# Performance work log

Hardware: AMD Instinct MI355X
Metric: run time of the kernel (lower is better)

Reference implementation:

```python
import jax, jax.numpy as jnp
import numpy as np

N_HEADS = 8
TANH_CLIP = 10.0


def setup_inputs() -> dict:
    key = jax.random.key(0)
    ks = jax.random.split(key, 7)
    B, N, D = 128, 1000, 512
    embeddings = jax.random.normal(ks[0], (B, N, D), dtype=jnp.float32)
    step_context = jax.random.normal(ks[1], (B, 1, 2 * D), dtype=jnp.float32)
    # action mask: True = feasible action; guarantee at least one feasible per row
    action_mask = jax.random.uniform(ks[2], (B, 1, N)) > 0.3
    action_mask = action_mask.at[:, :, 0].set(True)
    s = 0.02
    W_node = jax.random.normal(ks[3], (D, 3 * D), dtype=jnp.float32) * s
    W_fixed = jax.random.normal(ks[4], (D, D), dtype=jnp.float32) * s
    W_step = jax.random.normal(ks[5], (2 * D, D), dtype=jnp.float32) * s
    W_out = jax.random.normal(ks[6], (D, D), dtype=jnp.float32) * s
    return {"embeddings": embeddings, "step_context": step_context,
            "action_mask": action_mask, "W_node": W_node, "W_fixed": W_fixed,
            "W_step": W_step, "W_out": W_out}


def reference(embeddings, step_context, action_mask, W_node, W_fixed, W_step, W_out):
    B, N, D = embeddings.shape
    H = N_HEADS
    hd = D // H
    neg_inf = jnp.float32(-jnp.inf)

    # --- precompute (Decoder._precompute) ---
    graph_embed = embeddings.mean(axis=1)                      # [B, D]
    kvl = embeddings @ W_node                                  # [B, N, 3D]
    _gk, gv, logit_key = jnp.split(kvl, 3, axis=-1)
    # source bug: glimpse_key variable is overwritten with glimpse_val, and
    # attention is called with key = value = glimpse_val
    KV = gv.reshape(B, N, H, hd).transpose(0, 2, 1, 3)         # [B, H, N, hd]
    graph_context = (graph_embed @ W_fixed)[:, None, :]        # [B, 1, D]

    # --- per-step query (Decoder._get_log_p) ---
    query = graph_context + step_context @ W_step              # [B, 1, D]
    q = query.reshape(B, 1, H, hd).transpose(0, 2, 1, 3)       # [B, H, 1, hd]

    # --- inner MHA (scaled_dot_product_attention with boolean mask) ---
    scores = jnp.einsum('bhqs,bhns->bhqn', q, KV) / jnp.sqrt(jnp.float32(hd))
    scores = jnp.where(action_mask[:, None, :, :], scores, neg_inf)  # [B,H,1,N]
    attn = jax.nn.softmax(scores, axis=-1)
    heads = jnp.einsum('bhqn,bhns->bhqs', attn, KV)            # [B, H, 1, hd]
    heads = heads.transpose(0, 2, 1, 3).reshape(B, 1, D)       # [B, 1, D]

    # --- glimpse projection and logit head ---
    glimpse = heads @ W_out                                    # [B, 1, D]
    logits = jnp.einsum('bqd,bnd->bqn', glimpse, logit_key) / jnp.sqrt(jnp.float32(D))
    logits = jnp.tanh(logits) * TANH_CLIP
    logits = jnp.where(action_mask, logits, neg_inf)
    return jax.nn.log_softmax(logits, axis=-1)                 # [B, 1, N]
```

## Files before the change

kernel.cpp:

```cpp
#include <hip/hip_runtime.h>
#include <math.h>

#define B 128
#define N 1000
#define D 512
#define H 8
#define NCHUNK 8
#define CHUNK 125
#define CG_N 10
#define SUBR 25
#define NSUB 4
#define ESW 516

#define OFF_PMEAN   0
#define OFF_QW      (OFF_PMEAN + B*NCHUNK*D)
#define OFF_PAE     (OFF_QW + B*D*H)
#define OFF_MC      (OFF_PAE + B*CG_N*H*D)
#define OFF_ZC      (OFF_MC + B*CG_N*H)
#define OFF_GW      (OFF_ZC + B*CG_N*H)
#define OFF_LG      (OFF_GW + B*D)
#define OFF_LMAX    (OFF_LG + B*N)
#define OFF_LSUM    (OFF_LMAX + B*NCHUNK)

__global__ void k1_partial_mean(const float* __restrict__ emb, float* __restrict__ ws){
    int chunk = blockIdx.x, b = blockIdx.y, t = threadIdx.x;
    const float4* e4 = (const float4*)emb;
    float4 acc = make_float4(0.f, 0.f, 0.f, 0.f);
    size_t rowbase = ((size_t)b * N + (size_t)chunk * CHUNK) * (D / 4);
    for (int n = 0; n < CHUNK; ++n) {
        float4 v = e4[rowbase + (size_t)n * (D / 4) + t];
        acc.x += v.x; acc.y += v.y; acc.z += v.z; acc.w += v.w;
    }
    float4* o = (float4*)(ws + OFF_PMEAN + (size_t)(b * NCHUNK + chunk) * D);
    o[t] = acc;
}

__global__ void k2_prep(const float* __restrict__ stepc, const float* __restrict__ Wnode,
                        const float* __restrict__ Wfix, const float* __restrict__ Wstep,
                        float* __restrict__ ws){
    int b = blockIdx.x, d = threadIdx.x;
    __shared__ float ge[D];
    __shared__ float q[D];
    float s = 0.f;
    #pragma unroll
    for (int c = 0; c < NCHUNK; ++c) s += ws[OFF_PMEAN + (size_t)(b * NCHUNK + c) * D + d];
    ge[d] = s * (1.0f / N);
    __syncthreads();
    float a0 = 0.f, a1 = 0.f, a2 = 0.f, a3 = 0.f;
    for (int k = 0; k < D; k += 4) {
        a0 = fmaf(ge[k],     Wfix[(size_t)k * D + d],       a0);
        a1 = fmaf(ge[k + 1], Wfix[(size_t)(k + 1) * D + d], a1);
        a2 = fmaf(ge[k + 2], Wfix[(size_t)(k + 2) * D + d], a2);
        a3 = fmaf(ge[k + 3], Wfix[(size_t)(k + 3) * D + d], a3);
    }
    const float* sc = stepc + (size_t)b * 2 * D;
    for (int k = 0; k < 2 * D; k += 4) {
        a0 = fmaf(sc[k],     Wstep[(size_t)k * D + d],       a0);
        a1 = fmaf(sc[k + 1], Wstep[(size_t)(k + 1) * D + d], a1);
        a2 = fmaf(sc[k + 2], Wstep[(size_t)(k + 2) * D + d], a2);
        a3 = fmaf(sc[k + 3], Wstep[(size_t)(k + 3) * D + d], a3);
    }
    q[d] = (a0 + a1) + (a2 + a3);
    __syncthreads();
    const float* wrow = Wnode + (size_t)d * 3 * D + D;
    float* outp = ws + OFF_QW + ((size_t)b * D + d) * H;
    #pragma unroll
    for (int h = 0; h < H; ++h) {
        float a = 0.f;
        const float* qh = q + h * 64;
        const float* wh = wrow + h * 64;
        #pragma unroll 8
        for (int s2 = 0; s2 < 64; ++s2) a = fmaf(qh[s2], wh[s2], a);
        outp[h] = a;
    }
}

__global__ __launch_bounds__(512) void kc_attn(const float* __restrict__ emb,
        const unsigned char* __restrict__ mask, float* __restrict__ ws){
    const int cg = blockIdx.x, b = blockIdx.y, t = threadIdx.x;
    __shared__ float es[SUBR * ESW];
    __shared__ float ps[16 * H * 32];
    __shared__ float sc[H * 32];
    __shared__ float pp[H * 32];
    __shared__ float mrun[H], zrun[H], ff[H];
    float acc[H];
    #pragma unroll
    for (int h = 0; h < H; ++h) acc[h] = 0.f;
    if (t < H) { mrun[t] = -INFINITY; zrun[t] = 0.f; }
    __syncthreads();
    const float* qw = ws + OFF_QW + (size_t)b * D * H;
    const int n_b = t & 31, dblk = t >> 5;
    for (int sub = 0; sub < NSUB; ++sub) {
        const int row0 = cg * (NSUB * SUBR) + sub * SUBR;
        const float4* e4 = (const float4*)(emb + ((size_t)b * N + row0) * D);
        #pragma unroll
        for (int r = 0; r < 7; ++r) {
            int idx = r * 512 + t;
            if (idx < SUBR * (D / 4)) {
                float4 v = e4[idx];
                int i = idx >> 7, c = idx & 127;
                *(float4*)&es[i * ESW + c * 4] = v;
            }
        }
        __syncthreads();
        {
            float a[H];
            #pragma unroll
            for (int h = 0; h < H; ++h) a[h] = 0.f;
            if (n_b < SUBR) {
                const float* er = es + n_b * ESW + dblk * 32;
                const float* qd = qw + (size_t)(dblk * 32) * H;
                #pragma unroll 8
                for (int dd = 0; dd < 32; ++dd) {
                    float e = er[dd];
                    float4 q0 = *(const float4*)(qd + dd * 8);
                    float4 q1 = *(const float4*)(qd + dd * 8 + 4);
                    a[0] = fmaf(e, q0.x, a[0]); a[1] = fmaf(e, q0.y, a[1]);
                    a[2] = fmaf(e, q0.z, a[2]); a[3] = fmaf(e, q0.w, a[3]);
                    a[4] = fmaf(e, q1.x, a[4]); a[5] = fmaf(e, q1.y, a[5]);
                    a[6] = fmaf(e, q1.z, a[6]); a[7] = fmaf(e, q1.w, a[7]);
                }
            }
            #pragma unroll
            for (int h = 0; h < H; ++h) ps[(dblk * H + h) * 32 + n_b] = a[h];
        }
        __syncthreads();
        if (t < 256) {
            int h = t >> 5, n = t & 31;
            float s = -INFINITY;
            if (n < SUBR) {
                float v = 0.f;
                #pragma unroll
                for (int k = 0; k < 16; ++k) v += ps[(k * H + h) * 32 + n];
                bool m = mask[(size_t)b * N + row0 + n] != 0;
                s = m ? v * 0.125f : -INFINITY;
            }
            sc[h * 32 + n] = s;
        }
        __syncthreads();
        if (t < 256) {
            int h = t >> 5, j = t & 31;
            float v = sc[h * 32 + j];
            float gm = v;
            #pragma unroll
            for (int o = 16; o > 0; o >>= 1) gm = fmaxf(gm, __shfl_xor(gm, o));
            float mold = mrun[h];
            float mnew = fmaxf(mold, gm);
            float p = (mnew == -INFINITY) ? 0.f : __expf(v - mnew);
            pp[h * 32 + j] = p;
            float zc = p;
            #pragma unroll
            for (int o = 16; o > 0; o >>= 1) zc += __shfl_xor(zc, o);
            if (j == 0) {
                float f = (mnew == -INFINITY) ? 1.f : __expf(mold - mnew);
                ff[h] = f;
                mrun[h] = mnew;
                zrun[h] = zrun[h] * f + zc;
            }
        }
        __syncthreads();
        #pragma unroll
        for (int h = 0; h < H; ++h) acc[h] *= ff[h];
        for (int i = 0; i < SUBR; ++i) {
            float e = es[i * ESW + t];
            #pragma unroll
            for (int h = 0; h < H; ++h) acc[h] = fmaf(pp[h * 32 + i], e, acc[h]);
        }
        __syncthreads();
    }
    float* paeb = ws + OFF_PAE + (((size_t)b * CG_N + cg) * H) * (size_t)D;
    #pragma unroll
    for (int h = 0; h < H; ++h) paeb[(size_t)h * D + t] = acc[h];
    if (t < H) {
        ws[OFF_MC + ((size_t)b * CG_N + cg) * H + t] = mrun[t];
        ws[OFF_ZC + ((size_t)b * CG_N + cg) * H + t] = zrun[t];
    }
}

__global__ __launch_bounds__(512) void kd_post(const float* __restrict__ Wnode,
        const float* __restrict__ Wout, float* __restrict__ ws){
    int b = blockIdx.x, t = threadIdx.x;
    __shared__ float ae[H * D];
    __shared__ float heads[D];
    __shared__ float gl[D];
    __shared__ float wgt[CG_N * H], iZ[H];
    if (t < H) {
        float M = -INFINITY;
        for (int c = 0; c < CG_N; ++c)
            M = fmaxf(M, ws[OFF_MC + ((size_t)b * CG_N + c) * H + t]);
        float Z = 0.f;
        for (int c = 0; c < CG_N; ++c) {
            float m = ws[OFF_MC + ((size_t)b * CG_N + c) * H + t];
            float w = (m == -INFINITY) ? 0.f : __expf(m - M);
            wgt[c * H + t] = w;
            Z += w * ws[OFF_ZC + ((size_t)b * CG_N + c) * H + t];
        }
        iZ[t] = 1.0f / Z;
    }
    __syncthreads();
    #pragma unroll
    for (int h = 0; h < H; ++h) {
        float s = 0.f;
        #pragma unroll
        for (int c = 0; c < CG_N; ++c)
            s += wgt[c * H + h] * ws[OFF_PAE + (((size_t)b * CG_N + c) * H + h) * (size_t)D + t];
        ae[h * D + t] = s * iZ[h];
    }
    __syncthreads();
    {
        int h = t >> 6;
        const float* aeh = ae + h * D;
        const float* col = Wnode + 512 + t;
        float a0 = 0.f, a1 = 0.f, a2 = 0.f, a3 = 0.f;
        for (int d = 0; d < D; d += 4) {
            a0 = fmaf(aeh[d],     col[(size_t)d * (3 * D)],       a0);
            a1 = fmaf(aeh[d + 1], col[(size_t)(d + 1) * (3 * D)], a1);
            a2 = fmaf(aeh[d + 2], col[(size_t)(d + 2) * (3 * D)], a2);
            a3 = fmaf(aeh[d + 3], col[(size_t)(d + 3) * (3 * D)], a3);
        }
        heads[t] = (a0 + a1) + (a2 + a3);
    }
    __syncthreads();
    {
        float a0 = 0.f, a1 = 0.f, a2 = 0.f, a3 = 0.f;
        for (int d = 0; d < D; d += 4) {
            a0 = fmaf(heads[d],     Wout[(size_t)d * D + t],       a0);
            a1 = fmaf(heads[d + 1], Wout[(size_t)(d + 1) * D + t], a1);
            a2 = fmaf(heads[d + 2], Wout[(size_t)(d + 2) * D + t], a2);
            a3 = fmaf(heads[d + 3], Wout[(size_t)(d + 3) * D + t], a3);
        }
        gl[t] = (a0 + a1) + (a2 + a3);
    }
    __syncthreads();
    {
        const float* wrow = Wnode + (size_t)t * (3 * D) + 2 * D;
        float a0 = 0.f, a1 = 0.f, a2 = 0.f, a3 = 0.f;
        for (int e = 0; e < D; e += 4) {
            a0 = fmaf(gl[e],     wrow[e],     a0);
            a1 = fmaf(gl[e + 1], wrow[e + 1], a1);
            a2 = fmaf(gl[e + 2], wrow[e + 2], a2);
            a3 = fmaf(gl[e + 3], wrow[e + 3], a3);
        }
        ws[OFF_GW + (size_t)b * D + t] = (a0 + a1) + (a2 + a3);
    }
}

__global__ void k7_logits(const float* __restrict__ emb, const unsigned char* __restrict__ mask,
                          float* __restrict__ ws){
    int chunk = blockIdx.x, b = blockIdx.y, t = threadIdx.x;
    __shared__ float4 gw4[D / 4];
    __shared__ float rmax[2], rsum[2];
    gw4[t] = ((const float4*)(ws + OFF_GW + (size_t)b * D))[t];
    __syncthreads();
    float lg = -INFINITY;
    int n = chunk * CHUNK + t;
    if (t < CHUNK) {
        const float4* e4 = (const float4*)(emb + ((size_t)b * N + n) * D);
        float a0 = 0.f, a1 = 0.f, a2 = 0.f, a3 = 0.f;
        for (int d4 = 0; d4 < D / 4; ++d4) {
            float4 e = e4[d4];
            float4 g = gw4[d4];
            a0 = fmaf(e.x, g.x, a0); a1 = fmaf(e.y, g.y, a1);
            a2 = fmaf(e.z, g.z, a2); a3 = fmaf(e.w, g.w, a3);
        }
        float accv = (a0 + a1) + (a2 + a3);
        bool m = mask[(size_t)b * N + n] != 0;
        lg = m ? tanhf(accv * 0.044194173824159216f) * 10.0f : -INFINITY;
        ws[OFF_LG + (size_t)b * N + n] = lg;
    }
    float mx = lg;
    #pragma unroll
    for (int o = 32; o > 0; o >>= 1) mx = fmaxf(mx, __shfl_xor(mx, o));
    if ((t & 63) == 0) rmax[t >> 6] = mx;
    __syncthreads();
    float bm = fmaxf(rmax[0], rmax[1]);
    float term = (lg == -INFINITY) ? 0.f : __expf(lg - bm);
    #pragma unroll
    for (int o = 32; o > 0; o >>= 1) term += __shfl_xor(term, o);
    if ((t & 63) == 0) rsum[t >> 6] = term;
    __syncthreads();
    if (t == 0) {
        ws[OFF_LMAX + (size_t)b * NCHUNK + chunk] = bm;
        ws[OFF_LSUM + (size_t)b * NCHUNK + chunk] = rsum[0] + rsum[1];
    }
}

__global__ void k8_out(const float* __restrict__ ws, float* __restrict__ out){
    int b = blockIdx.x, t = threadIdx.x;
    __shared__ float Ls;
    if (t == 0) {
        float M = -INFINITY;
        #pragma unroll
        for (int c = 0; c < NCHUNK; ++c)
            M = fmaxf(M, ws[OFF_LMAX + (size_t)b * NCHUNK + c]);
        float S = 0.f;
        #pragma unroll
        for (int c = 0; c < NCHUNK; ++c) {
            float m = ws[OFF_LMAX + (size_t)b * NCHUNK + c];
            if (m != -INFINITY) S += __expf(m - M) * ws[OFF_LSUM + (size_t)b * NCHUNK + c];
        }
        Ls = M + __logf(S);
    }
    __syncthreads();
    float L = Ls;
    for (int j = t; j < N; j += 256)
        out[(size_t)b * N + j] = fmaxf(ws[OFF_LG + (size_t)b * N + j] - L, -1e30f);
}

extern "C" void kernel_launch(void* const* d_in, const int* in_sizes, int n_in,
                              void* d_out, int out_size, void* d_ws, size_t ws_size,
                              hipStream_t stream) {
    const float* emb   = (const float*)d_in[0];
    const float* stepc = (const float*)d_in[1];
    const unsigned char* mask = (const unsigned char*)d_in[2];
    const float* Wnode = (const float*)d_in[3];
    const float* Wfix  = (const float*)d_in[4];
    const float* Wstep = (const float*)d_in[5];
    const float* Wout  = (const float*)d_in[6];
    float* out = (float*)d_out;
    float* ws  = (float*)d_ws;

    k1_partial_mean<<<dim3(NCHUNK, B), 128, 0, stream>>>(emb, ws);
    k2_prep<<<dim3(B), 512, 0, stream>>>(stepc, Wnode, Wfix, Wstep, ws);
    kc_attn<<<dim3(CG_N, B), 512, 0, stream>>>(emb, mask, ws);
    kd_post<<<dim3(B), 512, 0, stream>>>(Wnode, Wout, ws);
    k7_logits<<<dim3(NCHUNK, B), 128, 0, stream>>>(emb, mask, ws);
    k8_out<<<dim3(B), 256, 0, stream>>>(ws, out);
}
```

Baseline: 418.8 us.

## Replace online-softmax attention kernel with max-free two-pass chunked kernel

The tiled attention kernel (10 row groups, 25-row LDS sub-tiles, running max and rescaling) is replaced by a 128-thread kernel per 125-row chunk. Each thread computes one row's 8 head scores straight from global memory against LDS-cached query weights. It then exponentiates without subtracting a max, and a second pass re-reads the chunk to accumulate weighted embeddings. This drops the max bookkeeping, the rescaling and many barriers, and simplifies the merge in the post kernel. In exchange it reads embedding rows with a large per-thread stride, reads the chunk twice, and can overflow the exponent if scores are large.

```diff
diff --git a/kernel.cpp b/kernel.cpp
--- a/kernel.cpp
+++ b/kernel.cpp
@@ -7,17 +7,12 @@
 #define H 8
 #define NCHUNK 8
 #define CHUNK 125
-#define CG_N 10
-#define SUBR 25
-#define NSUB 4
-#define ESW 516
 
 #define OFF_PMEAN   0
 #define OFF_QW      (OFF_PMEAN + B*NCHUNK*D)
 #define OFF_PAE     (OFF_QW + B*D*H)
-#define OFF_MC      (OFF_PAE + B*CG_N*H*D)
-#define OFF_ZC      (OFF_MC + B*CG_N*H)
-#define OFF_GW      (OFF_ZC + B*CG_N*H)
+#define OFF_ZC      (OFF_PAE + B*NCHUNK*H*D)
+#define OFF_GW      (OFF_ZC + B*NCHUNK*H)
 #define OFF_LG      (OFF_GW + B*D)
 #define OFF_LMAX    (OFF_LG + B*N)
 #define OFF_LSUM    (OFF_LMAX + B*NCHUNK)
@@ -75,105 +70,75 @@
     }
 }
 
-__global__ __launch_bounds__(512) void kc_attn(const float* __restrict__ emb,
+__global__ __launch_bounds__(128) void kc2_attn(const float* __restrict__ emb,
         const unsigned char* __restrict__ mask, float* __restrict__ ws){
     const int cg = blockIdx.x, b = blockIdx.y, t = threadIdx.x;
-    __shared__ float es[SUBR * ESW];
-    __shared__ float ps[16 * H * 32];
-    __shared__ float sc[H * 32];
-    __shared__ float pp[H * 32];
-    __shared__ float mrun[H], zrun[H], ff[H];
-    float acc[H];
-    #pragma unroll
-    for (int h = 0; h < H; ++h) acc[h] = 0.f;
-    if (t < H) { mrun[t] = -INFINITY; zrun[t] = 0.f; }
-    __syncthreads();
-    const float* qw = ws + OFF_QW + (size_t)b * D * H;
-    const int n_b = t & 31, dblk = t >> 5;
-    for (int sub = 0; sub < NSUB; ++sub) {
-        const int row0 = cg * (NSUB * SUBR) + sub * SUBR;
-        const float4* e4 = (const float4*)(emb + ((size_t)b * N + row0) * D);
-        #pragma unroll
-        for (int r = 0; r < 7; ++r) {
-            int idx = r * 512 + t;
-            if (idx < SUBR * (D / 4)) {
-                float4 v = e4[idx];
-                int i = idx >> 7, c = idx & 127;
-                *(float4*)&es[i * ESW + c * 4] = v;
-            }
-        }
-        __syncthreads();
-        {
-            float a[H];
-            #pragma unroll
-            for (int h = 0; h < H; ++h) a[h] = 0.f;
-            if (n_b < SUBR) {
-                const float* er = es + n_b * ESW + dblk * 32;
-                const float* qd = qw + (size_t)(dblk * 32) * H;
-                #pragma unroll 8
-                for (int dd = 0; dd < 32; ++dd) {
-                    float e = er[dd];
-                    float4 q0 = *(const float4*)(qd + dd * 8);
-                    float4 q1 = *(const float4*)(qd + dd * 8 + 4);
-                    a[0] = fmaf(e, q0.x, a[0]); a[1] = fmaf(e, q0.y, a[1]);
-                    a[2] = fmaf(e, q0.z, a[2]); a[3] = fmaf(e, q0.w, a[3]);
-                    a[4] = fmaf(e, q1.x, a[4]); a[5] = fmaf(e, q1.y, a[5]);
-                    a[6] = fmaf(e, q1.z, a[6]); a[7] = fmaf(e, q1.w, a[7]);
+    __shared__ float qws[D * H];
+    __shared__ float p[H][128];
+    {
+        const float4* qg = (const float4*)(ws + OFF_QW + (size_t)b * D * H);
+        float4* qs4 = (float4*)qws;
+        #pragma unroll
+        for (int i = 0; i < 8; ++i) qs4[i * 128 + t] = qg[i * 128 + t];
+    }
+    __syncthreads();
+    {
+        float a[H];
+        #pragma unroll
+        for (int h = 0; h < H; ++h) a[h] = 0.f;
+        if (t < CHUNK) {
+            const int n = cg * CHUNK + t;
+            const float4* e4 = (const float4*)(emb + ((size_t)b * N + n) * D);
+            for (int d4 = 0; d4 < D / 4; ++d4) {
+                float4 e = e4[d4];
+                #pragma unroll
+                for (int j = 0; j < 4; ++j) {
+                    float ev = (j == 0) ? e.x : (j == 1) ? e.y : (j == 2) ? e.z : e.w;
+                    const float4* qp = (const float4*)&qws[(d4 * 4 + j) * H];
+                    float4 q0 = qp[0], q1 = qp[1];
+                    a[0] = fmaf(ev, q0.x, a[0]); a[1] = fmaf(ev, q0.y, a[1]);
+                    a[2] = fmaf(ev, q0.z, a[2]); a[3] = fmaf(ev, q0.w, a[3]);
+                    a[4] = fmaf(ev, q1.x, a[4]); a[5] = fmaf(ev, q1.y, a[5]);
+                    a[6] = fmaf(ev, q1.z, a[6]); a[7] = fmaf(ev, q1.w, a[7]);
                 }
             }
+            bool m = mask[(size_t)b * N + n] != 0;
             #pragma unroll
-            for (int h = 0; h < H; ++h) ps[(dblk * H + h) * 32 + n_b] = a[h];
-        }
-        __syncthreads();
-        if (t < 256) {
-            int h = t >> 5, n = t & 31;
-            float s = -INFINITY;
-            if (n < SUBR) {
-                float v = 0.f;
-                #pragma unroll
-                for (int k = 0; k < 16; ++k) v += ps[(k * H + h) * 32 + n];
-                bool m = mask[(size_t)b * N + row0 + n] != 0;
-                s = m ? v * 0.125f : -INFINITY;
+            for (int h = 0; h < H; ++h)
+                p[h][t] = m ? __expf(a[h] * 0.125f) : 0.f;
+        } else {
+            #pragma unroll
+            for (int h = 0; h < H; ++h) p[h][t] = 0.f;
+        }
+    }
+    __syncthreads();
+    {
+        int h = t >> 4, j = t & 15;
+        float z = 0.f;
+        for (int i = j; i < 128; i += 16) z += p[h][i];
+        #pragma unroll
+        for (int o = 8; o > 0; o >>= 1) z += __shfl_xor(z, o);
+        if (j == 0) ws[OFF_ZC + ((size_t)b * NCHUNK + cg) * H + h] = z;
+    }
+    {
+        float4 acc[H];
+        #pragma unroll
+        for (int h = 0; h < H; ++h) acc[h] = make_float4(0.f, 0.f, 0.f, 0.f);
+        const float4* ecol = (const float4*)(emb + ((size_t)b * N + (size_t)cg * CHUNK) * D) + t;
+        for (int i = 0; i < CHUNK; ++i) {
+            float4 e = ecol[(size_t)i * (D / 4)];
+            #pragma unroll
+            for (int h = 0; h < H; ++h) {
+                float w = p[h][i];
+                acc[h].x = fmaf(w, e.x, acc[h].x);
+                acc[h].y = fmaf(w, e.y, acc[h].y);
+                acc[h].z = fmaf(w, e.z, acc[h].z);
+                acc[h].w = fmaf(w, e.w, acc[h].w);
             }
-            sc[h * 32 + n] = s;
-        }
-        __syncthreads();
-        if (t < 256) {
-            int h = t >> 5, j = t & 31;
-            float v = sc[h * 32 + j];
-            float gm = v;
-            #pragma unroll
-            for (int o = 16; o > 0; o >>= 1) gm = fmaxf(gm, __shfl_xor(gm, o));
-            float mold = mrun[h];
-            float mnew = fmaxf(mold, gm);
-            float p = (mnew == -INFINITY) ? 0.f : __expf(v - mnew);
-            pp[h * 32 + j] = p;
-            float zc = p;
-            #pragma unroll
-            for (int o = 16; o > 0; o >>= 1) zc += __shfl_xor(zc, o);
-            if (j == 0) {
-                float f = (mnew == -INFINITY) ? 1.f : __expf(mold - mnew);
-                ff[h] = f;
-                mrun[h] = mnew;
-                zrun[h] = zrun[h] * f + zc;
-            }
-        }
-        __syncthreads();
-        #pragma unroll
-        for (int h = 0; h < H; ++h) acc[h] *= ff[h];
-        for (int i = 0; i < SUBR; ++i) {
-            float e = es[i * ESW + t];
-            #pragma unroll
-            for (int h = 0; h < H; ++h) acc[h] = fmaf(pp[h * 32 + i], e, acc[h]);
-        }
-        __syncthreads();
-    }
-    float* paeb = ws + OFF_PAE + (((size_t)b * CG_N + cg) * H) * (size_t)D;
-    #pragma unroll
-    for (int h = 0; h < H; ++h) paeb[(size_t)h * D + t] = acc[h];
-    if (t < H) {
-        ws[OFF_MC + ((size_t)b * CG_N + cg) * H + t] = mrun[t];
-        ws[OFF_ZC + ((size_t)b * CG_N + cg) * H + t] = zrun[t];
+        }
+        float4* paeb = (float4*)(ws + OFF_PAE + (((size_t)b * NCHUNK + cg) * H) * (size_t)D);
+        #pragma unroll
+        for (int h = 0; h < H; ++h) paeb[(size_t)h * (D / 4) + t] = acc[h];
     }
 }
 
@@ -183,18 +148,12 @@
     __shared__ float ae[H * D];
     __shared__ float heads[D];
     __shared__ float gl[D];
-    __shared__ float wgt[CG_N * H], iZ[H];
+    __shared__ float iZ[H];
     if (t < H) {
-        float M = -INFINITY;
-        for (int c = 0; c < CG_N; ++c)
-            M = fmaxf(M, ws[OFF_MC + ((size_t)b * CG_N + c) * H + t]);
         float Z = 0.f;
-        for (int c = 0; c < CG_N; ++c) {
-            float m = ws[OFF_MC + ((size_t)b * CG_N + c) * H + t];
-            float w = (m == -INFINITY) ? 0.f : __expf(m - M);
-            wgt[c * H + t] = w;
-            Z += w * ws[OFF_ZC + ((size_t)b * CG_N + c) * H + t];
-        }
+        #pragma unroll
+        for (int c = 0; c < NCHUNK; ++c)
+            Z += ws[OFF_ZC + ((size_t)b * NCHUNK + c) * H + t];
         iZ[t] = 1.0f / Z;
     }
     __syncthreads();
@@ -202,8 +161,8 @@
     for (int h = 0; h < H; ++h) {
         float s = 0.f;
         #pragma unroll
-        for (int c = 0; c < CG_N; ++c)
-            s += wgt[c * H + h] * ws[OFF_PAE + (((size_t)b * CG_N + c) * H + h) * (size_t)D + t];
+        for (int c = 0; c < NCHUNK; ++c)
+            s += ws[OFF_PAE + (((size_t)b * NCHUNK + c) * H + h) * (size_t)D + t];
         ae[h * D + t] = s * iZ[h];
     }
     __syncthreads();
@@ -322,7 +281,7 @@
 
     k1_partial_mean<<<dim3(NCHUNK, B), 128, 0, stream>>>(emb, ws);
     k2_prep<<<dim3(B), 512, 0, stream>>>(stepc, Wnode, Wfix, Wstep, ws);
-    kc_attn<<<dim3(CG_N, B), 512, 0, stream>>>(emb, mask, ws);
+    kc2_attn<<<dim3(NCHUNK, B), 128, 0, stream>>>(emb, mask, ws);
     kd_post<<<dim3(B), 512, 0, stream>>>(Wnode, Wout, ws);
     k7_logits<<<dim3(NCHUNK, B), 128, 0, stream>>>(emb, mask, ws);
     k8_out<<<dim3(B), 256, 0, stream>>>(ws, out);
```

Result: faster. 350.2 us (-16.4%).
